# Performance work log

Measured on AMD Instinct MI355X. Metric: run time of the kernel, lower is better.

The kernel has to match this reference:

```python
import math
import jax, jax.numpy as jnp
import numpy as np

B, S, D_MODEL, D_PROJ, N_ATTNS, NUM_CLASSES = 64, 300, 1024, 128, 4, 3862


def setup_inputs() -> dict:
    key = jax.random.key(0)
    ks = jax.random.split(key, 12)
    s = 1.0 / math.sqrt(D_MODEL)
    inp = {
        "seg_features": jax.random.normal(ks[0], (B, S, D_MODEL), dtype=jnp.float32),
        # per-head query linears (stacked): [H, d_proj, d_model]
        "Wq": jax.random.uniform(ks[1], (N_ATTNS, D_PROJ, D_MODEL), minval=-s, maxval=s, dtype=jnp.float32),
        "bq": jax.random.uniform(ks[2], (N_ATTNS, D_PROJ), minval=-s, maxval=s, dtype=jnp.float32),
        "Wk": jax.random.uniform(ks[3], (D_PROJ, D_MODEL), minval=-s, maxval=s, dtype=jnp.float32),
        "bk": jax.random.uniform(ks[4], (D_PROJ,), minval=-s, maxval=s, dtype=jnp.float32),
        "Wv": jax.random.uniform(ks[5], (D_PROJ, D_MODEL), minval=-s, maxval=s, dtype=jnp.float32),
        "bv": jax.random.uniform(ks[6], (D_PROJ,), minval=-s, maxval=s, dtype=jnp.float32),
        # conv1d(in=1, out=num_classes, kernel=d_proj) == linear [num_classes, d_proj]
        "Wc": jax.random.uniform(ks[7], (NUM_CLASSES, D_PROJ), minval=-1/math.sqrt(D_PROJ), maxval=1/math.sqrt(D_PROJ), dtype=jnp.float32),
        "bc": jax.random.uniform(ks[8], (NUM_CLASSES,), minval=-1/math.sqrt(D_PROJ), maxval=1/math.sqrt(D_PROJ), dtype=jnp.float32),
        "ln_a": jnp.ones((NUM_CLASSES,), dtype=jnp.float32),
        "ln_b": jnp.zeros((NUM_CLASSES,), dtype=jnp.float32),
    }
    return inp


def _layernorm(x, a, b, eps=1e-6):
    # torch LayerNorm variant: unbiased std, divide by (std + eps)
    mean = jnp.mean(x, axis=-1, keepdims=True)
    var = jnp.sum((x - mean) ** 2, axis=-1, keepdims=True) / (x.shape[-1] - 1)
    std = jnp.sqrt(var)
    return a * (x - mean) / (std + eps) + b


def reference(seg_features, Wq, bq, Wk, bk, Wv, bv, Wc, bc, ln_a, ln_b):
    scale = 1.0 / math.sqrt(D_PROJ)
    keys = jnp.einsum('bsd,pd->bsp', seg_features, Wk) + bk      # [B,S,P]
    vals = jnp.einsum('bsd,pd->bsp', seg_features, Wv) + bv      # [B,S,P]
    # all heads at once
    q = jnp.einsum('bsd,hpd->bhsp', seg_features, Wq) + bq[None, :, None, :]  # [B,H,S,P]
    score = jnp.einsum('bhsp,bsp->bhs', q, keys) * scale          # [B,H,S]
    p_attn = jax.nn.softmax(score, axis=-1)                       # [B,H,S]
    ws = jnp.einsum('bhs,bsp->bhp', p_attn, vals)                 # [B,H,P]
    logits = jnp.einsum('bhp,cp->bhc', jnp.maximum(ws, 0.0), Wc) + bc  # [B,H,C]
    logits = _layernorm(logits, ln_a, ln_b)                       # [B,H,C]
    logits = jnp.transpose(logits, (0, 2, 1))                     # [B,C,H]
    vid_logits = jnp.max(logits, axis=-1)                         # [B,C]
    attn_idc = jnp.argmax(logits, axis=-1)                        # [B,C]
    vid_probs = jax.nn.sigmoid(vid_logits)
    scores = jnp.transpose(score, (0, 2, 1))                      # [B,S,H]
    attn_weights = jnp.transpose(p_attn, (0, 2, 1))               # [B,S,H]
    # conv regularizer: conv applied to ones [B,1,P]
    conv_pars = jnp.sum(Wc, axis=-1)[None, :] + bc[None, :]       # [B? -> broadcast] -> [1,C]
    conv_pars = jnp.broadcast_to(conv_pars, (seg_features.shape[0], NUM_CLASSES))
    conv_pars = jax.nn.softmax(conv_pars, axis=1)
    mean_cp = jnp.mean(conv_pars, axis=1, keepdims=True)
    std_cp = jnp.sqrt(jnp.sum((conv_pars - mean_cp) ** 2, axis=1) / (NUM_CLASSES - 1))
    conv_loss = jnp.sum(jnp.clip(std_cp, 1e-9, 1e9), axis=0)
    return (vid_probs, attn_idc, scores, attn_weights, conv_loss)
```

## Files before the change

### kernel.cpp

```cpp
#include <hip/hip_runtime.h>
#include <math.h>

#define BATCH 64
#define SEQ 300
#define DM 1024
#define DP 128
#define NH 4
#define NC 3862
#define MROWS (BATCH*SEQ)
#define NSTK (6*DP)

#define BM 128
#define BN 128
#define BK 16

typedef double d4 __attribute__((ext_vector_type(4)));

__global__ __launch_bounds__(256, 2) void proj_gemm_mfma(
    const float* __restrict__ X,
    const float* __restrict__ Wk, const float* __restrict__ bk,
    const float* __restrict__ Wv, const float* __restrict__ bv,
    const float* __restrict__ Wq, const float* __restrict__ bq,
    float* __restrict__ O)
{
    const int mtile = blockIdx.x;
    const int wsel  = blockIdx.y;

    const float* Wbase; const float* bias;
    if (wsel == 0)      { Wbase = Wk; bias = bk; }
    else if (wsel == 1) { Wbase = Wv; bias = bv; }
    else                { Wbase = Wq + (size_t)(wsel - 2) * DP * DM;
                          bias  = bq + (wsel - 2) * DP; }

    __shared__ float As[2][BM * BK];
    __shared__ float Bs[2][BN * BK];

    const int tid  = threadIdx.x;
    const int lane = tid & 63;
    const int wave = tid >> 6;
    const int wm = wave >> 1, wn = wave & 1;
    const int mbase = mtile * BM;

    const int r = lane & 15;
    const int g = lane >> 4;
    const int sw = (r >> 2) & 3;

    d4 acc[4][4];
    #pragma unroll
    for (int mt = 0; mt < 4; ++mt)
        #pragma unroll
        for (int nt = 0; nt < 4; ++nt)
            acc[mt][nt] = (d4)(0.0);

#define STAGE(bufi, k0)                                                        \
    do {                                                                       \
        _Pragma("unroll")                                                      \
        for (int j = 0; j < 2; ++j) {                                          \
            const int slotbase = wave * 128 + j * 64;        \
            const int slot = slotbase + lane;                                  \
            const int mrow = slot >> 2;                                        \
            const int kq4  = (((slot & 3) ^ ((mrow >> 2) & 3))) << 2;          \
            const float* srcA = &X[(size_t)(mbase + mrow) * DM + (k0) + kq4];  \
            __builtin_amdgcn_global_load_lds(                                  \
                (const __attribute__((address_space(1))) void*)srcA,           \
                (__attribute__((address_space(3))) void*)&As[bufi][slotbase * 4], \
                16, 0, 0);                                                     \
            const float* srcB = &Wbase[(size_t)mrow * DM + (k0) + kq4];        \
            __builtin_amdgcn_global_load_lds(                                  \
                (const __attribute__((address_space(1))) void*)srcB,           \
                (__attribute__((address_space(3))) void*)&Bs[bufi][slotbase * 4], \
                16, 0, 0);                                                     \
        }                                                                      \
    } while (0)

    STAGE(0, 0);
    __syncthreads();

    int buf = 0;
    for (int t = 0; t < DM / BK; ++t) {
        if (t + 1 < DM / BK) {
            if (buf == 0) STAGE(1, (t + 1) * BK);
            else          STAGE(0, (t + 1) * BK);
        }
        #pragma unroll
        for (int kq = 0; kq < 4; ++kq) {
            const int kqs = ((kq ^ sw) << 2) + g;
            double a[4], b[4];
            #pragma unroll
            for (int mt = 0; mt < 4; ++mt)
                a[mt] = (double)As[buf][(wm * 64 + mt * 16 + r) * BK + kqs];
            #pragma unroll
            for (int nt = 0; nt < 4; ++nt)
                b[nt] = (double)Bs[buf][(wn * 64 + nt * 16 + r) * BK + kqs];
            #pragma unroll
            for (int mt = 0; mt < 4; ++mt)
                #pragma unroll
                for (int nt = 0; nt < 4; ++nt)
                    acc[mt][nt] = __builtin_amdgcn_mfma_f64_16x16x4f64(
                        a[mt], b[nt], acc[mt][nt], 0, 0, 0);
        }
        __syncthreads();
        buf ^= 1;
    }
#undef STAGE

    #pragma unroll
    for (int nt = 0; nt < 4; ++nt) {
        const int col = wn * 64 + nt * 16 + r;
        const double bi = (double)bias[col];
        #pragma unroll
        for (int mt = 0; mt < 4; ++mt) {
            #pragma unroll
            for (int i = 0; i < 4; ++i) {
                const int row = wm * 64 + mt * 16 + g + 4 * i;
                O[(size_t)(mbase + row) * NSTK + wsel * DP + col] =
                    (float)(acc[mt][nt][i] + bi);
            }
        }
    }
}

__global__ __launch_bounds__(256) void attn_kernel(
    const float* __restrict__ QKV,
    float* __restrict__ scores_out,
    float* __restrict__ attnw_out,
    double* __restrict__ wsrelu)
{
    const int b = blockIdx.x >> 2;
    const int h = blockIdx.x & 3;
    const int tid = threadIdx.x;
    const int wave = tid >> 6, lane = tid & 63;

    __shared__ double sc[SEQ];
    __shared__ double red[4];
    __shared__ double wacc[2][DP];

    const double scale = 0.08838834764831843;
    const float* base = QKV + (size_t)b * SEQ * NSTK;

    for (int s = wave; s < SEQ; s += 4) {
        const float* row = base + (size_t)s * NSTK;
        const float2 qv = *reinterpret_cast<const float2*>(row + 256 + h * DP + lane * 2);
        const float2 kv = *reinterpret_cast<const float2*>(row + lane * 2);
        double p = (double)qv.x * (double)kv.x + (double)qv.y * (double)kv.y;
        #pragma unroll
        for (int o = 32; o; o >>= 1) p += __shfl_xor(p, o);
        p *= scale;
        if (lane == 0) {
            sc[s] = p;
            scores_out[((size_t)b * SEQ + s) * NH + h] = (float)p;
        }
    }
    __syncthreads();

    double mx = -1e300;
    for (int i = tid; i < SEQ; i += 256) mx = fmax(mx, sc[i]);
    #pragma unroll
    for (int o = 32; o; o >>= 1) mx = fmax(mx, __shfl_xor(mx, o));
    if (lane == 0) red[wave] = mx;
    __syncthreads();
    mx = fmax(fmax(red[0], red[1]), fmax(red[2], red[3]));
    __syncthreads();

    double lsum = 0.0;
    for (int i = tid; i < SEQ; i += 256) {
        const double e = exp(sc[i] - mx);
        sc[i] = e;
        lsum += e;
    }
    #pragma unroll
    for (int o = 32; o; o >>= 1) lsum += __shfl_xor(lsum, o);
    if (lane == 0) red[wave] = lsum;
    __syncthreads();
    const double inv = 1.0 / (red[0] + red[1] + red[2] + red[3]);
    __syncthreads();
    for (int i = tid; i < SEQ; i += 256) {
        const double p = sc[i] * inv;
        sc[i] = p;
        attnw_out[((size_t)b * SEQ + i) * NH + h] = (float)p;
    }
    __syncthreads();

    const int p_idx = tid & 127, half = tid >> 7;
    double acc = 0.0;
    for (int s = half; s < SEQ; s += 2)
        acc = fma(sc[s], (double)base[(size_t)s * NSTK + 128 + p_idx], acc);
    wacc[half][p_idx] = acc;
    __syncthreads();
    if (tid < DP) {
        const double w = wacc[0][tid] + wacc[1][tid];
        wsrelu[((size_t)b * NH + h) * DP + tid] = fmax(w, 0.0);
    }
}

__global__ __launch_bounds__(256) void logits_kernel(
    const double* __restrict__ wsrelu, const float* __restrict__ Wc,
    const float* __restrict__ bc, double* __restrict__ logits,
    double* __restrict__ stats)
{
    const int bh = blockIdx.x;
    const int tid = threadIdx.x;
    const int wave = tid >> 6, lane = tid & 63;
    __shared__ double w4s[DP];
    __shared__ double red[4];
    if (tid < DP) w4s[tid] = wsrelu[(size_t)bh * DP + tid];
    __syncthreads();

    double lsum = 0.0;
    for (int c = tid; c < NC; c += 256) {
        const float4* wr = reinterpret_cast<const float4*>(Wc + (size_t)c * DP);
        double acc = 0.0;
        #pragma unroll
        for (int k = 0; k < 32; ++k) {
            const float4 v = wr[k];
            acc = fma((double)v.x, w4s[4 * k + 0], acc);
            acc = fma((double)v.y, w4s[4 * k + 1], acc);
            acc = fma((double)v.z, w4s[4 * k + 2], acc);
            acc = fma((double)v.w, w4s[4 * k + 3], acc);
        }
        acc += (double)bc[c];
        logits[(size_t)bh * NC + c] = acc;
        lsum += acc;
    }
    #pragma unroll
    for (int o = 32; o; o >>= 1) lsum += __shfl_xor(lsum, o);
    if (lane == 0) red[wave] = lsum;
    __syncthreads();
    const double mean = (red[0] + red[1] + red[2] + red[3]) / (double)NC;
    __syncthreads();

    double lss = 0.0;
    for (int c = tid; c < NC; c += 256) {
        const double d = logits[(size_t)bh * NC + c] - mean;
        lss = fma(d, d, lss);
    }
    #pragma unroll
    for (int o = 32; o; o >>= 1) lss += __shfl_xor(lss, o);
    if (lane == 0) red[wave] = lss;
    __syncthreads();
    if (tid == 0) {
        const double var = (red[0] + red[1] + red[2] + red[3]) / (double)(NC - 1);
        stats[bh * 2 + 0] = mean;
        stats[bh * 2 + 1] = sqrt(var);
    }
}

__global__ __launch_bounds__(256) void finalize_kernel(
    const double* __restrict__ logits, const double* __restrict__ stats,
    const float* __restrict__ ln_a, const float* __restrict__ ln_b,
    float* __restrict__ vid_probs, float* __restrict__ attn_idc)
{
    const int c = blockIdx.x * 256 + threadIdx.x;
    const int b = blockIdx.y;
    if (c >= NC) return;
    const double a = (double)ln_a[c], bb = (double)ln_b[c];
    double best = -1e300;
    int bi = 0;
    #pragma unroll
    for (int h = 0; h < NH; ++h) {
        const int bh = b * NH + h;
        const double x = logits[(size_t)bh * NC + c];
        const double ln = a * (x - stats[bh * 2]) / (stats[bh * 2 + 1] + 1e-6) + bb;
        if (ln > best) { best = ln; bi = h; }
    }
    vid_probs[(size_t)b * NC + c] = (float)(1.0 / (1.0 + exp(-best)));
    attn_idc[(size_t)b * NC + c] = (float)bi;
}

__global__ __launch_bounds__(256) void convloss_kernel(
    const float* __restrict__ Wc, const float* __restrict__ bc,
    float* __restrict__ out)
{
    __shared__ double t[NC];
    __shared__ double red[4];
    const int tid = threadIdx.x;
    const int wave = tid >> 6, lane = tid & 63;

    double lmax = -1e300;
    for (int c = tid; c < NC; c += 256) {
        const float4* wr = reinterpret_cast<const float4*>(Wc + (size_t)c * DP);
        double acc = 0.0;
        #pragma unroll
        for (int k = 0; k < 32; ++k) {
            const float4 v = wr[k];
            acc += (double)v.x + (double)v.y + (double)v.z + (double)v.w;
        }
        acc += (double)bc[c];
        t[c] = acc;
        lmax = fmax(lmax, acc);
    }
    #pragma unroll
    for (int o = 32; o; o >>= 1) lmax = fmax(lmax, __shfl_xor(lmax, o));
    if (lane == 0) red[wave] = lmax;
    __syncthreads();
    const double mx = fmax(fmax(red[0], red[1]), fmax(red[2], red[3]));
    __syncthreads();

    double lsum = 0.0;
    for (int c = tid; c < NC; c += 256) {
        const double e = exp(t[c] - mx);
        t[c] = e;
        lsum += e;
    }
    #pragma unroll
    for (int o = 32; o; o >>= 1) lsum += __shfl_xor(lsum, o);
    if (lane == 0) red[wave] = lsum;
    __syncthreads();
    const double inv = 1.0 / (red[0] + red[1] + red[2] + red[3]);
    __syncthreads();

    double psum = 0.0;
    for (int c = tid; c < NC; c += 256) {
        const double p = t[c] * inv;
        t[c] = p;
        psum += p;
    }
    #pragma unroll
    for (int o = 32; o; o >>= 1) psum += __shfl_xor(psum, o);
    if (lane == 0) red[wave] = psum;
    __syncthreads();
    const double mean = (red[0] + red[1] + red[2] + red[3]) / (double)NC;
    __syncthreads();

    double lss = 0.0;
    for (int c = tid; c < NC; c += 256) {
        const double d = t[c] - mean;
        lss = fma(d, d, lss);
    }
    #pragma unroll
    for (int o = 32; o; o >>= 1) lss += __shfl_xor(lss, o);
    if (lane == 0) red[wave] = lss;
    __syncthreads();
    if (tid == 0) {
        double stdv = sqrt((red[0] + red[1] + red[2] + red[3]) / (double)(NC - 1));
        stdv = fmin(fmax(stdv, 1e-9), 1e9);
        out[0] = (float)((double)BATCH * stdv);
    }
}

extern "C" void kernel_launch(void* const* d_in, const int* in_sizes, int n_in,
                              void* d_out, int out_size, void* d_ws, size_t ws_size,
                              hipStream_t stream)
{
    (void)in_sizes; (void)n_in; (void)out_size; (void)ws_size;
    const float* seg  = (const float*)d_in[0];
    const float* Wq   = (const float*)d_in[1];
    const float* bq   = (const float*)d_in[2];
    const float* Wk   = (const float*)d_in[3];
    const float* bk   = (const float*)d_in[4];
    const float* Wv   = (const float*)d_in[5];
    const float* bv   = (const float*)d_in[6];
    const float* Wc   = (const float*)d_in[7];
    const float* bc   = (const float*)d_in[8];
    const float* ln_a = (const float*)d_in[9];
    const float* ln_b = (const float*)d_in[10];

    float* out = (float*)d_out;
    float* vid_probs = out;
    float* attn_idc  = out + (size_t)BATCH * NC;
    float* scores    = attn_idc + (size_t)BATCH * NC;
    float* attnw     = scores + (size_t)BATCH * SEQ * NH;
    float* convl     = attnw + (size_t)BATCH * SEQ * NH;

    char* wsp = (char*)d_ws;
    float*  QKV    = (float*)wsp;
    wsp += (size_t)MROWS * NSTK * sizeof(float);
    double* wsrelu = (double*)wsp;
    wsp += (size_t)BATCH * NH * DP * sizeof(double);
    double* logits = (double*)wsp;
    wsp += (size_t)BATCH * NH * NC * sizeof(double);
    double* stats  = (double*)wsp;

    dim3 g1(MROWS / BM, NSTK / BN);
    proj_gemm_mfma<<<g1, 256, 0, stream>>>(seg, Wk, bk, Wv, bv, Wq, bq, QKV);

    attn_kernel<<<BATCH * NH, 256, 0, stream>>>(QKV, scores, attnw, wsrelu);

    logits_kernel<<<BATCH * NH, 256, 0, stream>>>(wsrelu, Wc, bc, logits, stats);

    dim3 g3((NC + 255) / 256, BATCH);
    finalize_kernel<<<g3, 256, 0, stream>>>(logits, stats, ln_a, ln_b, vid_probs, attn_idc);

    convloss_kernel<<<1, 256, 0, stream>>>(Wc, bc, convl);
}
```

Baseline: 850.1 us.

## Fuse attention and logits kernels, widen blocks, raise GEMM occupancy hint

Merges the attention kernel and the logits/LayerNorm-stats kernel into one 512-thread kernel. The ReLU'd weighted sum stays in LDS, and logits are kept in registers for the variance pass, so the wsrelu round trip and the logits reread are gone. The score dot product now uses 16-lane groups with float4 loads, and convloss runs with 1024 threads. The projection GEMM's launch-bounds occupancy hint rises from 2 to 4, which may force register spilling in the double-precision MFMA kernel.

```diff
diff --git a/kernel.cpp b/kernel.cpp
--- a/kernel.cpp
+++ b/kernel.cpp
@@ -16,7 +16,7 @@
 
 typedef double d4 __attribute__((ext_vector_type(4)));
 
-__global__ __launch_bounds__(256, 2) void proj_gemm_mfma(
+__global__ __launch_bounds__(256, 4) void proj_gemm_mfma(
     const float* __restrict__ X,
     const float* __restrict__ Wk, const float* __restrict__ bk,
     const float* __restrict__ Wv, const float* __restrict__ bv,
@@ -120,50 +120,67 @@
     }
 }
 
-__global__ __launch_bounds__(256) void attn_kernel(
+__global__ __launch_bounds__(512) void attn_logits_kernel(
     const float* __restrict__ QKV,
+    const float* __restrict__ Wc, const float* __restrict__ bc,
     float* __restrict__ scores_out,
     float* __restrict__ attnw_out,
-    double* __restrict__ wsrelu)
+    double* __restrict__ logits,
+    double* __restrict__ stats)
 {
     const int b = blockIdx.x >> 2;
     const int h = blockIdx.x & 3;
+    const int bh = blockIdx.x;
     const int tid = threadIdx.x;
     const int wave = tid >> 6, lane = tid & 63;
 
     __shared__ double sc[SEQ];
-    __shared__ double red[4];
-    __shared__ double wacc[2][DP];
+    __shared__ double red[8];
+    __shared__ double wacc[4][DP];
+    __shared__ double wsLDS[DP];
 
     const double scale = 0.08838834764831843;
     const float* base = QKV + (size_t)b * SEQ * NSTK;
 
-    for (int s = wave; s < SEQ; s += 4) {
-        const float* row = base + (size_t)s * NSTK;
-        const float2 qv = *reinterpret_cast<const float2*>(row + 256 + h * DP + lane * 2);
-        const float2 kv = *reinterpret_cast<const float2*>(row + lane * 2);
-        double p = (double)qv.x * (double)kv.x + (double)qv.y * (double)kv.y;
-        #pragma unroll
-        for (int o = 32; o; o >>= 1) p += __shfl_xor(p, o);
-        p *= scale;
-        if (lane == 0) {
-            sc[s] = p;
-            scores_out[((size_t)b * SEQ + s) * NH + h] = (float)p;
+    {
+        const int grp = tid >> 4;
+        const int l16 = tid & 15;
+        for (int s = grp; s < SEQ; s += 32) {
+            const float* row = base + (size_t)s * NSTK;
+            const float4 q0 = *reinterpret_cast<const float4*>(row + 256 + h * DP + l16 * 8);
+            const float4 q1 = *reinterpret_cast<const float4*>(row + 256 + h * DP + l16 * 8 + 4);
+            const float4 k0 = *reinterpret_cast<const float4*>(row + l16 * 8);
+            const float4 k1 = *reinterpret_cast<const float4*>(row + l16 * 8 + 4);
+            double p = (double)q0.x * (double)k0.x + (double)q0.y * (double)k0.y
+                     + (double)q0.z * (double)k0.z + (double)q0.w * (double)k0.w
+                     + (double)q1.x * (double)k1.x + (double)q1.y * (double)k1.y
+                     + (double)q1.z * (double)k1.z + (double)q1.w * (double)k1.w;
+            p += __shfl_xor(p, 1);
+            p += __shfl_xor(p, 2);
+            p += __shfl_xor(p, 4);
+            p += __shfl_xor(p, 8);
+            p *= scale;
+            if (l16 == 0) {
+                sc[s] = p;
+                scores_out[((size_t)b * SEQ + s) * NH + h] = (float)p;
+            }
         }
     }
     __syncthreads();
 
     double mx = -1e300;
-    for (int i = tid; i < SEQ; i += 256) mx = fmax(mx, sc[i]);
+    for (int i = tid; i < SEQ; i += 512) mx = fmax(mx, sc[i]);
     #pragma unroll
     for (int o = 32; o; o >>= 1) mx = fmax(mx, __shfl_xor(mx, o));
     if (lane == 0) red[wave] = mx;
     __syncthreads();
-    mx = fmax(fmax(red[0], red[1]), fmax(red[2], red[3]));
+    mx = red[0];
+    #pragma unroll
+    for (int w = 1; w < 8; ++w) mx = fmax(mx, red[w]);
     __syncthreads();
 
     double lsum = 0.0;
-    for (int i = tid; i < SEQ; i += 256) {
+    for (int i = tid; i < SEQ; i += 512) {
         const double e = exp(sc[i] - mx);
         sc[i] = e;
         lsum += e;
@@ -172,66 +189,64 @@
     for (int o = 32; o; o >>= 1) lsum += __shfl_xor(lsum, o);
     if (lane == 0) red[wave] = lsum;
     __syncthreads();
-    const double inv = 1.0 / (red[0] + red[1] + red[2] + red[3]);
-    __syncthreads();
-    for (int i = tid; i < SEQ; i += 256) {
+    double tot = 0.0;
+    #pragma unroll
+    for (int w = 0; w < 8; ++w) tot += red[w];
+    const double inv = 1.0 / tot;
+    __syncthreads();
+    for (int i = tid; i < SEQ; i += 512) {
         const double p = sc[i] * inv;
         sc[i] = p;
         attnw_out[((size_t)b * SEQ + i) * NH + h] = (float)p;
     }
     __syncthreads();
 
-    const int p_idx = tid & 127, half = tid >> 7;
-    double acc = 0.0;
-    for (int s = half; s < SEQ; s += 2)
-        acc = fma(sc[s], (double)base[(size_t)s * NSTK + 128 + p_idx], acc);
-    wacc[half][p_idx] = acc;
+    {
+        const int p_idx = tid & 127, qtr = tid >> 7;
+        double acc = 0.0;
+        for (int s = qtr; s < SEQ; s += 4)
+            acc = fma(sc[s], (double)base[(size_t)s * NSTK + 128 + p_idx], acc);
+        wacc[qtr][p_idx] = acc;
+    }
     __syncthreads();
     if (tid < DP) {
-        const double w = wacc[0][tid] + wacc[1][tid];
-        wsrelu[((size_t)b * NH + h) * DP + tid] = fmax(w, 0.0);
-    }
-}
-
-__global__ __launch_bounds__(256) void logits_kernel(
-    const double* __restrict__ wsrelu, const float* __restrict__ Wc,
-    const float* __restrict__ bc, double* __restrict__ logits,
-    double* __restrict__ stats)
-{
-    const int bh = blockIdx.x;
-    const int tid = threadIdx.x;
-    const int wave = tid >> 6, lane = tid & 63;
-    __shared__ double w4s[DP];
-    __shared__ double red[4];
-    if (tid < DP) w4s[tid] = wsrelu[(size_t)bh * DP + tid];
-    __syncthreads();
-
-    double lsum = 0.0;
-    for (int c = tid; c < NC; c += 256) {
+        const double w = wacc[0][tid] + wacc[1][tid] + wacc[2][tid] + wacc[3][tid];
+        wsLDS[tid] = fmax(w, 0.0);
+    }
+    __syncthreads();
+
+    double vals[8];
+    int cnt = 0;
+    double psum = 0.0;
+    for (int c = tid; c < NC; c += 512) {
         const float4* wr = reinterpret_cast<const float4*>(Wc + (size_t)c * DP);
         double acc = 0.0;
         #pragma unroll
         for (int k = 0; k < 32; ++k) {
             const float4 v = wr[k];
-            acc = fma((double)v.x, w4s[4 * k + 0], acc);
-            acc = fma((double)v.y, w4s[4 * k + 1], acc);
-            acc = fma((double)v.z, w4s[4 * k + 2], acc);
-            acc = fma((double)v.w, w4s[4 * k + 3], acc);
+            acc = fma((double)v.x, wsLDS[4 * k + 0], acc);
+            acc = fma((double)v.y, wsLDS[4 * k + 1], acc);
+            acc = fma((double)v.z, wsLDS[4 * k + 2], acc);
+            acc = fma((double)v.w, wsLDS[4 * k + 3], acc);
         }
         acc += (double)bc[c];
         logits[(size_t)bh * NC + c] = acc;
-        lsum += acc;
-    }
-    #pragma unroll
-    for (int o = 32; o; o >>= 1) lsum += __shfl_xor(lsum, o);
-    if (lane == 0) red[wave] = lsum;
-    __syncthreads();
-    const double mean = (red[0] + red[1] + red[2] + red[3]) / (double)NC;
+        vals[cnt++] = acc;
+        psum += acc;
+    }
+    #pragma unroll
+    for (int o = 32; o; o >>= 1) psum += __shfl_xor(psum, o);
+    if (lane == 0) red[wave] = psum;
+    __syncthreads();
+    double msum = 0.0;
+    #pragma unroll
+    for (int w = 0; w < 8; ++w) msum += red[w];
+    const double mean = msum / (double)NC;
     __syncthreads();
 
     double lss = 0.0;
-    for (int c = tid; c < NC; c += 256) {
-        const double d = logits[(size_t)bh * NC + c] - mean;
+    for (int i = 0; i < cnt; ++i) {
+        const double d = vals[i] - mean;
         lss = fma(d, d, lss);
     }
     #pragma unroll
@@ -239,9 +254,11 @@
     if (lane == 0) red[wave] = lss;
     __syncthreads();
     if (tid == 0) {
-        const double var = (red[0] + red[1] + red[2] + red[3]) / (double)(NC - 1);
+        double vsum = 0.0;
+        #pragma unroll
+        for (int w = 0; w < 8; ++w) vsum += red[w];
         stats[bh * 2 + 0] = mean;
-        stats[bh * 2 + 1] = sqrt(var);
+        stats[bh * 2 + 1] = sqrt(vsum / (double)(NC - 1));
     }
 }
 
@@ -267,17 +284,17 @@
     attn_idc[(size_t)b * NC + c] = (float)bi;
 }
 
-__global__ __launch_bounds__(256) void convloss_kernel(
+__global__ __launch_bounds__(1024) void convloss_kernel(
     const float* __restrict__ Wc, const float* __restrict__ bc,
     float* __restrict__ out)
 {
     __shared__ double t[NC];
-    __shared__ double red[4];
+    __shared__ double red[16];
     const int tid = threadIdx.x;
     const int wave = tid >> 6, lane = tid & 63;
 
     double lmax = -1e300;
-    for (int c = tid; c < NC; c += 256) {
+    for (int c = tid; c < NC; c += 1024) {
         const float4* wr = reinterpret_cast<const float4*>(Wc + (size_t)c * DP);
         double acc = 0.0;
         #pragma unroll
@@ -293,11 +310,13 @@
     for (int o = 32; o; o >>= 1) lmax = fmax(lmax, __shfl_xor(lmax, o));
     if (lane == 0) red[wave] = lmax;
     __syncthreads();
-    const double mx = fmax(fmax(red[0], red[1]), fmax(red[2], red[3]));
+    double mx = red[0];
+    #pragma unroll
+    for (int w = 1; w < 16; ++w) mx = fmax(mx, red[w]);
     __syncthreads();
 
     double lsum = 0.0;
-    for (int c = tid; c < NC; c += 256) {
+    for (int c = tid; c < NC; c += 1024) {
         const double e = exp(t[c] - mx);
         t[c] = e;
         lsum += e;
@@ -306,11 +325,14 @@
     for (int o = 32; o; o >>= 1) lsum += __shfl_xor(lsum, o);
     if (lane == 0) red[wave] = lsum;
     __syncthreads();
-    const double inv = 1.0 / (red[0] + red[1] + red[2] + red[3]);
+    double tot = 0.0;
+    #pragma unroll
+    for (int w = 0; w < 16; ++w) tot += red[w];
+    const double inv = 1.0 / tot;
     __syncthreads();
 
     double psum = 0.0;
-    for (int c = tid; c < NC; c += 256) {
+    for (int c = tid; c < NC; c += 1024) {
         const double p = t[c] * inv;
         t[c] = p;
         psum += p;
@@ -319,11 +341,14 @@
     for (int o = 32; o; o >>= 1) psum += __shfl_xor(psum, o);
     if (lane == 0) red[wave] = psum;
     __syncthreads();
-    const double mean = (red[0] + red[1] + red[2] + red[3]) / (double)NC;
+    double msum = 0.0;
+    #pragma unroll
+    for (int w = 0; w < 16; ++w) msum += red[w];
+    const double mean = msum / (double)NC;
     __syncthreads();
 
     double lss = 0.0;
-    for (int c = tid; c < NC; c += 256) {
+    for (int c = tid; c < NC; c += 1024) {
         const double d = t[c] - mean;
         lss = fma(d, d, lss);
     }
@@ -332,7 +357,10 @@
     if (lane == 0) red[wave] = lss;
     __syncthreads();
     if (tid == 0) {
-        double stdv = sqrt((red[0] + red[1] + red[2] + red[3]) / (double)(NC - 1));
+        double vsum = 0.0;
+        #pragma unroll
+        for (int w = 0; w < 16; ++w) vsum += red[w];
+        double stdv = sqrt(vsum / (double)(NC - 1));
         stdv = fmin(fmax(stdv, 1e-9), 1e9);
         out[0] = (float)((double)BATCH * stdv);
     }
@@ -365,8 +393,6 @@
     char* wsp = (char*)d_ws;
     float*  QKV    = (float*)wsp;
     wsp += (size_t)MROWS * NSTK * sizeof(float);
-    double* wsrelu = (double*)wsp;
-    wsp += (size_t)BATCH * NH * DP * sizeof(double);
     double* logits = (double*)wsp;
     wsp += (size_t)BATCH * NH * NC * sizeof(double);
     double* stats  = (double*)wsp;
@@ -374,12 +400,11 @@
     dim3 g1(MROWS / BM, NSTK / BN);
     proj_gemm_mfma<<<g1, 256, 0, stream>>>(seg, Wk, bk, Wv, bv, Wq, bq, QKV);
 
-    attn_kernel<<<BATCH * NH, 256, 0, stream>>>(QKV, scores, attnw, wsrelu);
-
-    logits_kernel<<<BATCH * NH, 256, 0, stream>>>(wsrelu, Wc, bc, logits, stats);
+    attn_logits_kernel<<<BATCH * NH, 512, 0, stream>>>(
+        QKV, Wc, bc, scores, attnw, logits, stats);
 
     dim3 g3((NC + 255) / 256, BATCH);
     finalize_kernel<<<g3, 256, 0, stream>>>(logits, stats, ln_a, ln_b, vid_probs, attn_idc);
 
-    convloss_kernel<<<1, 256, 0, stream>>>(Wc, bc, convl);
+    convloss_kernel<<<1, 1024, 0, stream>>>(Wc, bc, convl);
 }
```

After: 2.107 ms. +147.9%, slower.
